# Performance work log

Measured on AMD Instinct MI355X. Metric: run time of the kernel, lower is better.

## Reference

```python
import jax, jax.numpy as jnp
from jax import lax
import numpy as np

D_COND = 48      # d_condition
K = 24           # n_bins
HID = 128        # hidden_dim
T = 10           # n_transforms
TAIL = 15.0      # tail_bound
B = 131072       # batch (contexts x samples flattened, as in sample())


def setup_inputs() -> dict:
    key = jax.random.key(0)
    ks = jax.random.split(key, 8)
    def w(k, shape, fan_in, gain=1.0):
        return (jax.random.normal(k, shape, jnp.float32) * (gain / np.sqrt(fan_in))).astype(jnp.float32)
    return {
        "z": jax.random.normal(ks[0], (B,), jnp.float32),
        "context": jax.random.normal(ks[1], (B, D_COND), jnp.float32),
        "W0": w(ks[2], (T, D_COND, HID), D_COND),
        "b0": jnp.zeros((T, HID), jnp.float32),
        "W1": w(ks[3], (T, HID, HID), HID),
        "b1": jnp.zeros((T, HID), jnp.float32),
        "W2": w(ks[4], (T, HID, HID), HID),
        "b2": jnp.zeros((T, HID), jnp.float32),
        "W3": w(ks[5], (T, HID, 3 * K + 1), HID, gain=0.1),
        "b3": jnp.zeros((T, 3 * K + 1), jnp.float32),
        "loc": jnp.float32(85.0),
        "scale": jnp.float32(5.0),
    }


def _spline_forward(x, widths, heights, derivs):
    # x: (B,); widths/heights: (B,K); derivs: (B,K+1)
    inside = (x >= -TAIL) & (x <= TAIL)
    cw = jnp.pad(jnp.cumsum(widths, -1), ((0, 0), (1, 0)), constant_values=-TAIL)   # (B,K+1)
    ch = jnp.pad(jnp.cumsum(heights, -1), ((0, 0), (1, 0)), constant_values=-TAIL)  # (B,K+1)
    # torch.searchsorted(cw[...,1:], x, right=False) == count of elems < x
    idx = jnp.clip(jnp.sum(cw[:, 1:] < x[:, None], axis=-1), 0, K - 1)
    take = lambda a, i: jnp.take_along_axis(a, i[:, None], axis=-1)[:, 0]
    w_k = take(widths, idx)
    h_k = take(heights, idx)
    cw_k = take(cw, idx)
    ch_k = take(ch, idx)
    d_k = take(derivs, idx)
    d_k1 = take(derivs, idx + 1)
    s = h_k / w_k
    xi = jnp.clip((x - cw_k) / w_k, 1e-6, 1.0 - 1e-6)
    one_m = 1.0 - xi
    numer = h_k * (s * xi * xi + d_k * xi * one_m)
    denom = s + (d_k + d_k1 - 2.0 * s) * xi * one_m
    y = ch_k + numer / denom
    dy_dxi = s * s * (d_k1 * xi * xi + 2.0 * s * xi * one_m + d_k * one_m * one_m) / (denom * denom)
    log_det = (jnp.log(jnp.maximum(dy_dxi, 1e-10))
               + jnp.log(jnp.maximum(h_k, 1e-10))
               - jnp.log(jnp.maximum(w_k, 1e-10)))
    y = jnp.where(inside, y, x)
    log_det = jnp.where(inside, log_det, 0.0)
    return y, log_det


def reference(z, context, W0, b0, W1, b1, W2, b2, W3, b3, loc, scale):
    def body(carry, p):
        zc, ld = carry
        w0, c0, w1, c1, w2, c2, w3, c3 = p
        h = jax.nn.silu(context @ w0 + c0)
        h = jax.nn.silu(h @ w1 + c1)
        h = jax.nn.silu(h @ w2 + c2)
        params = h @ w3 + c3                                   # (B, 3K+1)
        Wl, Hl, Dl = params[:, :K], params[:, K:2 * K], params[:, 2 * K:]
        widths = jax.nn.softmax(Wl, axis=-1) * (2.0 * TAIL)
        heights = jax.nn.softmax(Hl, axis=-1) * (2.0 * TAIL)
        derivs = jax.nn.softplus(Dl) + 1e-3
        y, l = _spline_forward(zc, widths, heights, derivs)
        return (y, ld + l), None

    (z_out, total_ld), _ = lax.scan(body, (z, jnp.zeros_like(z)),
                                    (W0, b0, W1, b1, W2, b2, W3, b3))
    s = jnp.maximum(scale, 0.1)
    temp_f = z_out * s + loc   # _unstandardize, as in sample()
    return temp_f, total_ld
```

## Files before the change

kernel.cpp:

```cpp
#include <hip/hip_runtime.h>
#include <hip/hip_bf16.h>

#define DCOND 48
#define KBINS 24
#define HID 128
#define TSTEPS 10
#define NPAR 73
#define TAILF 15.0f

typedef __attribute__((ext_vector_type(8))) short v8s;
typedef __attribute__((ext_vector_type(4))) float f32x4;
typedef __attribute__((ext_vector_type(4))) unsigned u32x4;

__device__ __forceinline__ short f2bf(float f) {
    __hip_bfloat16 h = __float2bfloat16(f);
    return __builtin_bit_cast(short, h);
}
__device__ __forceinline__ float bf2f(short s) {
    unsigned u = ((unsigned)(unsigned short)s) << 16;
    return __builtin_bit_cast(float, u);
}
__device__ __forceinline__ float silu_f(float v) {
    return __fdividef(v, 1.0f + __expf(-v));
}

__device__ __forceinline__ unsigned cvt_pk(float a, float b) {
    unsigned r;
    asm("v_cvt_pk_bf16_f32 %0, %1, %2" : "=v"(r) : "v"(a), "v"(b));
    return r;
}

__device__ __forceinline__ void split8(f32x4 a0, f32x4 a1, v8s& hi, v8s& lo) {
    unsigned h0 = cvt_pk(a0[0], a0[1]);
    unsigned h1 = cvt_pk(a0[2], a0[3]);
    unsigned h2 = cvt_pk(a1[0], a1[1]);
    unsigned h3 = cvt_pk(a1[2], a1[3]);
    float l0 = a0[0] - __builtin_bit_cast(float, h0 << 16);
    float l1 = a0[1] - __builtin_bit_cast(float, h0 & 0xffff0000u);
    float l2 = a0[2] - __builtin_bit_cast(float, h1 << 16);
    float l3 = a0[3] - __builtin_bit_cast(float, h1 & 0xffff0000u);
    float l4 = a1[0] - __builtin_bit_cast(float, h2 << 16);
    float l5 = a1[1] - __builtin_bit_cast(float, h2 & 0xffff0000u);
    float l6 = a1[2] - __builtin_bit_cast(float, h3 << 16);
    float l7 = a1[3] - __builtin_bit_cast(float, h3 & 0xffff0000u);
    unsigned q0 = cvt_pk(l0, l1);
    unsigned q1 = cvt_pk(l2, l3);
    unsigned q2 = cvt_pk(l4, l5);
    unsigned q3 = cvt_pk(l6, l7);
    hi = __builtin_bit_cast(v8s, (u32x4){h0, h1, h2, h3});
    lo = __builtin_bit_cast(v8s, (u32x4){q0, q1, q2, q3});
}

__global__ void prep_w(const float* __restrict__ W0, const float* __restrict__ W1,
                       const float* __restrict__ W2, const float* __restrict__ W3,
                       short* __restrict__ ws)
{
    int g = blockIdx.x * 256 + threadIdx.x;
    if (g >= TSTEPS * 102400) return;
    int t = g / 102400;
    int o = g % 102400;

    int base, NT, Kreal, Nreal, Nstr;
    const float* W;
    if (o < 16384)      { base = 0;     NT = 8; Kreal = 48;  Nreal = 128; Nstr = 128;  W = W0 + (size_t)t * DCOND * HID; }
    else if (o < 49152) { base = 16384; NT = 8; Kreal = 128; Nreal = 128; Nstr = 128;  W = W1 + (size_t)t * HID * HID; }
    else if (o < 81920) { base = 49152; NT = 8; Kreal = 128; Nreal = 128; Nstr = 128;  W = W2 + (size_t)t * HID * HID; }
    else                { base = 81920; NT = 5; Kreal = 128; Nreal = 73;  Nstr = NPAR; W = W3 + (size_t)t * HID * NPAR; }

    int r     = o - base;
    int psz   = 2 * NT * 512;
    int kc    = r / psz;
    int rem   = r % psz;
    int plane = rem / (NT * 512);
    int e     = rem % (NT * 512);
    int nt = e >> 9;
    int ln = (e >> 3) & 63;
    int j  = e & 7;
    int k  = kc * 32 + (ln >> 4) * 8 + j;
    int n  = nt * 16 + (ln & 15);

    float v = 0.0f;
    if (k < Kreal && n < Nreal) v = W[(size_t)k * Nstr + n];
    short hi = f2bf(v);
    ws[(size_t)t * 102400 + o] = plane ? f2bf(v - bf2f(hi)) : hi;
}

#define MBLK 64
#define NTHR 256

template<int SHORTS>
__device__ __forceinline__ void stage_piece(const short* __restrict__ g,
                                            short* lds, int tid)
{
    constexpr int R = (SHORTS + 2047) / 2048;
    const int wuni = (tid >> 6) << 9;
    #pragma unroll
    for (int i = 0; i < R; ++i) {
        const int so = i * 2048 + tid * 8;
        if ((SHORTS % 2048 == 0) || so < SHORTS)
            __builtin_amdgcn_global_load_lds(
                (const __attribute__((address_space(1))) void*)(g + so),
                (__attribute__((address_space(3))) void*)(lds + i * 2048 + wuni),
                16, 0, 0);
    }
}

template<int NT>
__device__ __forceinline__ void init_acc(f32x4* acc, const float* __restrict__ bias,
                                         int nreal, int lane)
{
    const int ncol = lane & 15;
    #pragma unroll
    for (int nt = 0; nt < NT; ++nt) {
        const int n = nt * 16 + ncol;
        const float bv = (n < nreal) ? bias[n] : 0.0f;
        acc[nt] = (f32x4){bv, bv, bv, bv};
    }
}

template<int NT>
__device__ __forceinline__ void mfma_piece(f32x4* acc, const short* __restrict__ buf,
                                           v8s ah, v8s al, int lane)
{
    const short* bb = buf + lane * 8;
    #pragma unroll
    for (int nt = 0; nt < NT; ++nt) {
        v8s bh = *(const v8s*)(bb + nt * 512);
        v8s bl = *(const v8s*)(bb + (NT + nt) * 512);
        acc[nt] = __builtin_amdgcn_mfma_f32_16x16x32_bf16(ah, bh, acc[nt], 0, 0, 0);
        acc[nt] = __builtin_amdgcn_mfma_f32_16x16x32_bf16(al, bh, acc[nt], 0, 0, 0);
        acc[nt] = __builtin_amdgcn_mfma_f32_16x16x32_bf16(ah, bl, acc[nt], 0, 0, 0);
    }
}

template<int NT, bool ACT>
__device__ __forceinline__ void cwrite(const f32x4* acc, float* __restrict__ Hlds,
                                       int lane, int wave)
{
    const int ncol  = lane & 15;
    const int crow0 = wave * 16 + (lane >> 4) * 4;
    #pragma unroll
    for (int nt = 0; nt < NT; ++nt) {
        #pragma unroll
        for (int r = 0; r < 4; ++r) {
            const int row = crow0 + r;
            const int sw  = (row & 7) << 4;
            float v = acc[nt][r];
            if (ACT) v = silu_f(v);
            *(float*)((char*)Hlds + row * 512 + ((((nt * 16 + ncol)) * 4) ^ sw)) = v;
        }
    }
}

__device__ __forceinline__ void a_split4(const float* __restrict__ Hlds,
                                         int arow, int asw, int lane,
                                         v8s (&ah)[4], v8s (&al)[4])
{
    const int kg = (lane >> 4) * 8;
    const char* hr = (const char*)Hlds + arow * 512;
    #pragma unroll
    for (int kc = 0; kc < 4; ++kc) {
        const int kb = (kc * 32 + kg) * 4;
        f32x4 a0 = *(const f32x4*)(hr + (kb ^ asw));
        f32x4 a1 = *(const f32x4*)(hr + ((kb + 16) ^ asw));
        split8(a0, a1, ah[kc], al[kc]);
    }
}

__global__ __launch_bounds__(NTHR, 2)
void nsf_mfma(const float* __restrict__ z_g, const float* __restrict__ ctx_g,
              const float* __restrict__ b0g, const float* __restrict__ b1g,
              const float* __restrict__ b2g, const float* __restrict__ b3g,
              const float* __restrict__ locp, const float* __restrict__ sclp,
              const short* __restrict__ wsW, float* __restrict__ out, int B)
{
    __shared__ float Hlds[MBLK * 128];
    __shared__ short CtxH[MBLK * 64];
    __shared__ short CtxL[MBLK * 64];
    __shared__ short Wbuf[2][8192];
    const int tid  = threadIdx.x;
    const int lane = tid & 63, wave = tid >> 6;
    const int blk  = blockIdx.x;

    stage_piece<8192>(wsW, Wbuf[0], tid);

    {
        const int row = tid >> 2, q = tid & 3;
        const int sw  = (row & 7) << 4;
        v8s h0, l0, h1, l1;
        if (q < 3) {
            int gs = blk * MBLK + row;
            if (gs > B - 1) gs = B - 1;
            const float* cg = ctx_g + (size_t)gs * DCOND + q * 16;
            f32x4 c0 = *(const f32x4*)cg;
            f32x4 c1 = *(const f32x4*)(cg + 4);
            f32x4 c2 = *(const f32x4*)(cg + 8);
            f32x4 c3 = *(const f32x4*)(cg + 12);
            split8(c0, c1, h0, l0);
            split8(c2, c3, h1, l1);
        } else {
            #pragma unroll
            for (int u = 0; u < 8; ++u) { h0[u] = 0; l0[u] = 0; h1[u] = 0; l1[u] = 0; }
        }
        char* ph = (char*)CtxH + row * 128;
        char* pl = (char*)CtxL + row * 128;
        *(v8s*)(ph + ((q * 32)      ^ sw)) = h0;
        *(v8s*)(ph + ((q * 32 + 16) ^ sw)) = h1;
        *(v8s*)(pl + ((q * 32)      ^ sw)) = l0;
        *(v8s*)(pl + ((q * 32 + 16) ^ sw)) = l1;
    }

    float x = 0.0f, ld = 0.0f;
    if (lane < 16) {
        int gid = blk * MBLK + wave * 16 + lane;
        if (gid > B - 1) gid = B - 1;
        x = z_g[gid];
    }

    __syncthreads();
    int cur = 0;

    const int arow = wave * 16 + (lane & 15);
    const int asw  = (arow & 7) << 4;

    v8s ah[4], al[4];
    f32x4 acc[8];

#define SLOT(STAGE_SHORTS, STAGE_SRC, NT_, AH, AL)                         \
    stage_piece<STAGE_SHORTS>((STAGE_SRC), Wbuf[cur ^ 1], tid);            \
    mfma_piece<NT_>(acc, Wbuf[cur], (AH), (AL), lane);

    #pragma unroll 1
    for (int t = 0; t < TSTEPS; ++t) {
        const short* ws0 = wsW + (size_t)t * 102400;
        const short* wsn = wsW + (size_t)((t + 1) % TSTEPS) * 102400;
        const float* b0 = b0g + t * HID;
        const float* b1 = b1g + t * HID;
        const float* b2 = b2g + t * HID;
        const float* b3 = b3g + t * NPAR;

        {
            const char* ph = (const char*)CtxH + arow * 128;
            const char* pl = (const char*)CtxL + arow * 128;
            const int kg2 = (lane >> 4) * 16;
            ah[0] = *(const v8s*)(ph + ((kg2)      ^ asw));
            al[0] = *(const v8s*)(pl + ((kg2)      ^ asw));
            ah[1] = *(const v8s*)(ph + ((64 + kg2) ^ asw));
            al[1] = *(const v8s*)(pl + ((64 + kg2) ^ asw));
        }
        init_acc<8>(acc, b0, HID, lane);
        SLOT(8192, ws0 + 8192,  8, ah[0], al[0]);  __syncthreads(); cur ^= 1;
        SLOT(8192, ws0 + 16384, 8, ah[1], al[1]);
        cwrite<8, true>(acc, Hlds, lane, wave);
        a_split4(Hlds, arow, asw, lane, ah, al);
        __syncthreads(); cur ^= 1;

        init_acc<8>(acc, b1, HID, lane);
        SLOT(8192, ws0 + 24576, 8, ah[0], al[0]);  __syncthreads(); cur ^= 1;
        SLOT(8192, ws0 + 32768, 8, ah[1], al[1]);  __syncthreads(); cur ^= 1;
        SLOT(8192, ws0 + 40960, 8, ah[2], al[2]);  __syncthreads(); cur ^= 1;
        SLOT(8192, ws0 + 49152, 8, ah[3], al[3]);
        cwrite<8, true>(acc, Hlds, lane, wave);
        a_split4(Hlds, arow, asw, lane, ah, al);
        __syncthreads(); cur ^= 1;

        init_acc<8>(acc, b2, HID, lane);
        SLOT(8192, ws0 + 57344, 8, ah[0], al[0]);  __syncthreads(); cur ^= 1;
        SLOT(8192, ws0 + 65536, 8, ah[1], al[1]);  __syncthreads(); cur ^= 1;
        SLOT(8192, ws0 + 73728, 8, ah[2], al[2]);  __syncthreads(); cur ^= 1;
        SLOT(5120, ws0 + 81920, 8, ah[3], al[3]);
        cwrite<8, true>(acc, Hlds, lane, wave);
        a_split4(Hlds, arow, asw, lane, ah, al);
        __syncthreads(); cur ^= 1;

        init_acc<5>(acc, b3, NPAR, lane);
        SLOT(5120, ws0 + 87040, 5, ah[0], al[0]);  __syncthreads(); cur ^= 1;
        SLOT(5120, ws0 + 92160, 5, ah[1], al[1]);  __syncthreads(); cur ^= 1;
        SLOT(5120, ws0 + 97280, 5, ah[2], al[2]);  __syncthreads(); cur ^= 1;
        SLOT(8192, wsn,         5, ah[3], al[3]);
        cwrite<5, false>(acc, Hlds, lane, wave);

        if (lane < 16) {
            const int srow = wave * 16 + lane;
            const char* hrow = (const char*)Hlds + srow * 512;
            const int sw = (srow & 7) << 4;

            float pw[KBINS], ph[KBINS];
            #pragma unroll
            for (int g = 0; g < 6; ++g) {
                f32x4 vw = *(const f32x4*)(hrow + ((g * 16) ^ sw));
                f32x4 vh = *(const f32x4*)(hrow + (((g + 6) * 16) ^ sw));
                #pragma unroll
                for (int u = 0; u < 4; ++u) { pw[g * 4 + u] = vw[u]; ph[g * 4 + u] = vh[u]; }
            }
            float mw = pw[0], mh = ph[0];
            #pragma unroll
            for (int i = 1; i < KBINS; ++i) { mw = fmaxf(mw, pw[i]); mh = fmaxf(mh, ph[i]); }
            float wsum = 0.0f, hsum = 0.0f;
            #pragma unroll
            for (int i = 0; i < KBINS; ++i) {
                pw[i] = __expf(pw[i] - mw); wsum += pw[i];
                ph[i] = __expf(ph[i] - mh); hsum += ph[i];
            }
            const float wmul = __fdividef(2.0f * TAILF, wsum);
            const float hmul = __fdividef(2.0f * TAILF, hsum);

            float cw = 0.0f, ch = 0.0f;
            float cwk = -TAILF, chk = -TAILF;
            float wk = pw[0] * wmul, hk = ph[0] * hmul;
            int idx = 0;
            #pragma unroll
            for (int i = 1; i < KBINS; ++i) {
                cw += pw[i - 1] * wmul;
                ch += ph[i - 1] * hmul;
                if (cw < x) {
                    cwk = cw; chk = ch;
                    wk = pw[i] * wmul; hk = ph[i] * hmul;
                    idx = i;
                }
            }
            float d0 = *(const float*)(hrow + (((2 * KBINS + idx) * 4) ^ sw));
            float d1 = *(const float*)(hrow + (((2 * KBINS + idx + 1) * 4) ^ sw));
            const float dk  = fmaxf(d0, 0.0f) + __logf(1.0f + __expf(-fabsf(d0))) + 0.001f;
            const float dk1 = fmaxf(d1, 0.0f) + __logf(1.0f + __expf(-fabsf(d1))) + 0.001f;

            const bool inside = (x >= -TAILF) && (x <= TAILF);
            const float sr = __fdividef(hk, wk);
            float xi = __fdividef(x - cwk, wk);
            xi = fminf(fmaxf(xi, 1e-6f), 1.0f - 1e-6f);
            const float om  = 1.0f - xi;
            const float xio = xi * om;
            const float numer = hk * (sr * xi * xi + dk * xio);
            const float denom = sr + (dk + dk1 - 2.0f * sr) * xio;
            const float y = chk + __fdividef(numer, denom);
            const float dyd = __fdividef(sr * sr * (dk1 * xi * xi + 2.0f * sr * xio + dk * om * om),
                                         denom * denom);
            const float lg = __logf(fmaxf(dyd, 1e-10f)) + __logf(fmaxf(hk, 1e-10f))
                           - __logf(fmaxf(wk, 1e-10f));
            x  = inside ? y : x;
            ld += inside ? lg : 0.0f;
        }
        __syncthreads(); cur ^= 1;
    }
#undef SLOT

    if (lane < 16) {
        const int gid = blk * MBLK + wave * 16 + lane;
        if (gid < B) {
            const float s = fmaxf(sclp[0], 0.1f);
            out[gid]     = fmaf(x, s, locp[0]);
            out[B + gid] = ld;
        }
    }
}

#define FBLK 256
template<int KIN, int WS, int NOUT, bool ACT>
__device__ __forceinline__ void dense_chunk(const float* __restrict__ W,
                                            const float* __restrict__ bias,
                                            int j0, const float (&hin)[KIN],
                                            float* __restrict__ sb, int tid)
{
    #pragma unroll 1
    for (int jj = 0; jj < NOUT; jj += 8) {
        const int j = j0 + jj;
        float a[8];
        #pragma unroll
        for (int u = 0; u < 8; ++u) a[u] = bias[j + u];
        #pragma unroll
        for (int k = 0; k < KIN; ++k) {
            const float* w = W + k * WS + j;
            const float hk = hin[k];
            #pragma unroll
            for (int u = 0; u < 8; ++u) a[u] = fmaf(hk, w[u], a[u]);
        }
        #pragma unroll
        for (int u = 0; u < 8; ++u) {
            float v = ACT ? silu_f(a[u]) : a[u];
            sb[(jj + u) * FBLK + tid] = v;
        }
    }
}

__global__ __launch_bounds__(FBLK, 2)
void nsf_fwd_slow(const float* __restrict__ z_g, const float* __restrict__ ctx_g,
                  const float* __restrict__ W0g, const float* __restrict__ b0g,
                  const float* __restrict__ W1g, const float* __restrict__ b1g,
                  const float* __restrict__ W2g, const float* __restrict__ b2g,
                  const float* __restrict__ W3g, const float* __restrict__ b3g,
                  const float* __restrict__ locp, const float* __restrict__ sclp,
                  float* __restrict__ out, int B)
{
    __shared__ float sbuf[64 * FBLK];
    const int tid = threadIdx.x;
    const int gid = blockIdx.x * FBLK + tid;
    if (gid >= B) return;
    float x = z_g[gid], ld = 0.0f;
    #pragma unroll 1
    for (int t = 0; t < TSTEPS; ++t) {
        asm volatile("" ::: "memory");
        const float* W0 = W0g + (size_t)t * DCOND * HID;
        const float* b0 = b0g + (size_t)t * HID;
        const float* W1 = W1g + (size_t)t * HID * HID;
        const float* b1 = b1g + (size_t)t * HID;
        const float* W2 = W2g + (size_t)t * HID * HID;
        const float* b2 = b2g + (size_t)t * HID;
        const float* W3 = W3g + (size_t)t * HID * NPAR;
        const float* b3 = b3g + (size_t)t * NPAR;
        float ctx[DCOND];
        #pragma unroll
        for (int k = 0; k < DCOND; ++k) ctx[k] = ctx_g[(size_t)gid * DCOND + k];
        float h[HID];
        dense_chunk<DCOND, HID, 64, true>(W0, b0, 0, ctx, sbuf, tid);
        #pragma unroll
        for (int j = 0; j < 64; ++j) h[j] = sbuf[j * FBLK + tid];
        dense_chunk<DCOND, HID, 64, true>(W0, b0, 64, ctx, sbuf, tid);
        #pragma unroll
        for (int j = 0; j < 64; ++j) h[64 + j] = sbuf[j * FBLK + tid];
        #pragma unroll 1
        for (int l = 0; l < 2; ++l) {
            const float* W  = (l == 0) ? W1 : W2;
            const float* bb = (l == 0) ? b1 : b2;
            float hlo[64];
            dense_chunk<HID, HID, 64, true>(W, bb, 0, h, sbuf, tid);
            #pragma unroll
            for (int j = 0; j < 64; ++j) hlo[j] = sbuf[j * FBLK + tid];
            dense_chunk<HID, HID, 64, true>(W, bb, 64, h, sbuf, tid);
            #pragma unroll
            for (int j = 0; j < 64; ++j) h[64 + j] = sbuf[j * FBLK + tid];
            #pragma unroll
            for (int j = 0; j < 64; ++j) h[j] = hlo[j];
        }
        float p[NPAR];
        dense_chunk<HID, NPAR, 64, false>(W3, b3, 0, h, sbuf, tid);
        #pragma unroll
        for (int j = 0; j < 64; ++j) p[j] = sbuf[j * FBLK + tid];
        dense_chunk<HID, NPAR, 8, false>(W3, b3, 64, h, sbuf, tid);
        #pragma unroll
        for (int j = 0; j < 8; ++j) p[64 + j] = sbuf[j * FBLK + tid];
        {
            float a = b3[72];
            #pragma unroll
            for (int k = 0; k < HID; ++k) a = fmaf(h[k], W3[k * NPAR + 72], a);
            p[72] = a;
        }
        float mw = p[0];
        #pragma unroll
        for (int i = 1; i < KBINS; ++i) mw = fmaxf(mw, p[i]);
        float we[KBINS]; float wsum = 0.0f;
        #pragma unroll
        for (int i = 0; i < KBINS; ++i) { we[i] = __expf(p[i] - mw); wsum += we[i]; }
        const float wmul = __fdividef(2.0f * TAILF, wsum);
        float mh = p[KBINS];
        #pragma unroll
        for (int i = 1; i < KBINS; ++i) mh = fmaxf(mh, p[KBINS + i]);
        float he[KBINS]; float hsum = 0.0f;
        #pragma unroll
        for (int i = 0; i < KBINS; ++i) { he[i] = __expf(p[KBINS + i] - mh); hsum += he[i]; }
        const float hmul = __fdividef(2.0f * TAILF, hsum);
        float dvv[KBINS + 1];
        #pragma unroll
        for (int i = 0; i <= KBINS; ++i) {
            float xd = p[2 * KBINS + i];
            dvv[i] = fmaxf(xd, 0.0f) + __logf(1.0f + __expf(-fabsf(xd))) + 0.001f;
        }
        float cw = 0.0f, ch = 0.0f, cwk = -TAILF, chk = -TAILF;
        float wk = we[0] * wmul, hk = he[0] * hmul, dk = dvv[0], dk1 = dvv[1];
        #pragma unroll
        for (int i = 1; i < KBINS; ++i) {
            cw += we[i - 1] * wmul;
            ch += he[i - 1] * hmul;
            if (cw < x) {
                cwk = cw; chk = ch;
                wk = we[i] * wmul; hk = he[i] * hmul;
                dk = dvv[i]; dk1 = dvv[i + 1];
            }
        }
        const bool inside = (x >= -TAILF) && (x <= TAILF);
        const float sr = __fdividef(hk, wk);
        float xi = __fdividef(x - cwk, wk);
        xi = fminf(fmaxf(xi, 1e-6f), 1.0f - 1e-6f);
        const float om  = 1.0f - xi;
        const float xio = xi * om;
        const float numer = hk * (sr * xi * xi + dk * xio);
        const float denom = sr + (dk + dk1 - 2.0f * sr) * xio;
        const float y = chk + __fdividef(numer, denom);
        const float dyd = __fdividef(sr * sr * (dk1 * xi * xi + 2.0f * sr * xio + dk * om * om),
                                     denom * denom);
        const float lg = __logf(fmaxf(dyd, 1e-10f)) + __logf(fmaxf(hk, 1e-10f))
                       - __logf(fmaxf(wk, 1e-10f));
        x  = inside ? y : x;
        ld += inside ? lg : 0.0f;
    }
    const float s = fmaxf(sclp[0], 0.1f);
    out[gid]     = fmaf(x, s, locp[0]);
    out[B + gid] = ld;
}

extern "C" void kernel_launch(void* const* d_in, const int* in_sizes, int n_in,
                              void* d_out, int out_size, void* d_ws, size_t ws_size,
                              hipStream_t stream) {
    const float* z    = (const float*)d_in[0];
    const float* ctx  = (const float*)d_in[1];
    const float* W0   = (const float*)d_in[2];
    const float* b0   = (const float*)d_in[3];
    const float* W1   = (const float*)d_in[4];
    const float* b1   = (const float*)d_in[5];
    const float* W2   = (const float*)d_in[6];
    const float* b2   = (const float*)d_in[7];
    const float* W3   = (const float*)d_in[8];
    const float* b3   = (const float*)d_in[9];
    const float* loc  = (const float*)d_in[10];
    const float* scl  = (const float*)d_in[11];
    float* out = (float*)d_out;
    const int B = in_sizes[0];

    const size_t ws_need = (size_t)TSTEPS * 102400 * sizeof(short);
    if (ws_size < ws_need) {
        const int nblk = (B + FBLK - 1) / FBLK;
        hipLaunchKernelGGL(nsf_fwd_slow, dim3(nblk), dim3(FBLK), 0, stream,
                           z, ctx, W0, b0, W1, b1, W2, b2, W3, b3, loc, scl, out, B);
        return;
    }

    short* ws = (short*)d_ws;
    const int prep_total = TSTEPS * 102400;
    hipLaunchKernelGGL(prep_w, dim3((prep_total + 255) / 256), dim3(256), 0, stream,
                       W0, W1, W2, W3, ws);

    const int nblk = (B + MBLK - 1) / MBLK;
    hipLaunchKernelGGL(nsf_mfma, dim3(nblk), dim3(NTHR), 0, stream,
                       z, ctx, b0, b1, b2, b3, loc, scl, ws, out, B);
}
```

Before: 678.1 us.

## Halve block rows and split N across wave pairs for higher occupancy

The row tile per block drops from 64 to 32. Each pair of waves now shares a 16-row M tile and splits the N columns in half, so every wave keeps 4 accumulators instead of 8. The weight staging buffer shrinks to 4096 shorts per stage and launch bounds ask for 4 blocks per CU, aiming at more resident blocks and fewer registers per thread. The cost is twice as many weight loads from global memory per sample, many more __syncthreads barriers with smaller pieces per stage, and an uneven N split in the last layer (4 tiles against 1).

```diff
diff --git a/kernel.cpp b/kernel.cpp
--- a/kernel.cpp
+++ b/kernel.cpp
@@ -85,7 +85,7 @@
     ws[(size_t)t * 102400 + o] = plane ? f2bf(v - bf2f(hi)) : hi;
 }
 
-#define MBLK 64
+#define MBLK 32
 #define NTHR 256
 
 template<int SHORTS>
@@ -105,69 +105,7 @@
     }
 }
 
-template<int NT>
-__device__ __forceinline__ void init_acc(f32x4* acc, const float* __restrict__ bias,
-                                         int nreal, int lane)
-{
-    const int ncol = lane & 15;
-    #pragma unroll
-    for (int nt = 0; nt < NT; ++nt) {
-        const int n = nt * 16 + ncol;
-        const float bv = (n < nreal) ? bias[n] : 0.0f;
-        acc[nt] = (f32x4){bv, bv, bv, bv};
-    }
-}
-
-template<int NT>
-__device__ __forceinline__ void mfma_piece(f32x4* acc, const short* __restrict__ buf,
-                                           v8s ah, v8s al, int lane)
-{
-    const short* bb = buf + lane * 8;
-    #pragma unroll
-    for (int nt = 0; nt < NT; ++nt) {
-        v8s bh = *(const v8s*)(bb + nt * 512);
-        v8s bl = *(const v8s*)(bb + (NT + nt) * 512);
-        acc[nt] = __builtin_amdgcn_mfma_f32_16x16x32_bf16(ah, bh, acc[nt], 0, 0, 0);
-        acc[nt] = __builtin_amdgcn_mfma_f32_16x16x32_bf16(al, bh, acc[nt], 0, 0, 0);
-        acc[nt] = __builtin_amdgcn_mfma_f32_16x16x32_bf16(ah, bl, acc[nt], 0, 0, 0);
-    }
-}
-
-template<int NT, bool ACT>
-__device__ __forceinline__ void cwrite(const f32x4* acc, float* __restrict__ Hlds,
-                                       int lane, int wave)
-{
-    const int ncol  = lane & 15;
-    const int crow0 = wave * 16 + (lane >> 4) * 4;
-    #pragma unroll
-    for (int nt = 0; nt < NT; ++nt) {
-        #pragma unroll
-        for (int r = 0; r < 4; ++r) {
-            const int row = crow0 + r;
-            const int sw  = (row & 7) << 4;
-            float v = acc[nt][r];
-            if (ACT) v = silu_f(v);
-            *(float*)((char*)Hlds + row * 512 + ((((nt * 16 + ncol)) * 4) ^ sw)) = v;
-        }
-    }
-}
-
-__device__ __forceinline__ void a_split4(const float* __restrict__ Hlds,
-                                         int arow, int asw, int lane,
-                                         v8s (&ah)[4], v8s (&al)[4])
-{
-    const int kg = (lane >> 4) * 8;
-    const char* hr = (const char*)Hlds + arow * 512;
-    #pragma unroll
-    for (int kc = 0; kc < 4; ++kc) {
-        const int kb = (kc * 32 + kg) * 4;
-        f32x4 a0 = *(const f32x4*)(hr + (kb ^ asw));
-        f32x4 a1 = *(const f32x4*)(hr + ((kb + 16) ^ asw));
-        split8(a0, a1, ah[kc], al[kc]);
-    }
-}
-
-__global__ __launch_bounds__(NTHR, 2)
+__global__ __launch_bounds__(NTHR, 4)
 void nsf_mfma(const float* __restrict__ z_g, const float* __restrict__ ctx_g,
               const float* __restrict__ b0g, const float* __restrict__ b1g,
               const float* __restrict__ b2g, const float* __restrict__ b3g,
@@ -177,111 +115,137 @@
     __shared__ float Hlds[MBLK * 128];
     __shared__ short CtxH[MBLK * 64];
     __shared__ short CtxL[MBLK * 64];
-    __shared__ short Wbuf[2][8192];
+    __shared__ short Wbuf[2][4096];
     const int tid  = threadIdx.x;
     const int lane = tid & 63, wave = tid >> 6;
+    const int mt   = wave >> 1, h = wave & 1;
     const int blk  = blockIdx.x;
 
-    stage_piece<8192>(wsW, Wbuf[0], tid);
+    stage_piece<4096>(wsW, Wbuf[0], tid);
 
     {
-        const int row = tid >> 2, q = tid & 3;
+        const int row = tid >> 3, q = tid & 7;
         const int sw  = (row & 7) << 4;
-        v8s h0, l0, h1, l1;
-        if (q < 3) {
+        v8s ch_, cl_;
+        if (q < 6) {
             int gs = blk * MBLK + row;
             if (gs > B - 1) gs = B - 1;
-            const float* cg = ctx_g + (size_t)gs * DCOND + q * 16;
+            const float* cg = ctx_g + (size_t)gs * DCOND + q * 8;
             f32x4 c0 = *(const f32x4*)cg;
             f32x4 c1 = *(const f32x4*)(cg + 4);
-            f32x4 c2 = *(const f32x4*)(cg + 8);
-            f32x4 c3 = *(const f32x4*)(cg + 12);
-            split8(c0, c1, h0, l0);
-            split8(c2, c3, h1, l1);
+            split8(c0, c1, ch_, cl_);
         } else {
             #pragma unroll
-            for (int u = 0; u < 8; ++u) { h0[u] = 0; l0[u] = 0; h1[u] = 0; l1[u] = 0; }
-        }
-        char* ph = (char*)CtxH + row * 128;
-        char* pl = (char*)CtxL + row * 128;
-        *(v8s*)(ph + ((q * 32)      ^ sw)) = h0;
-        *(v8s*)(ph + ((q * 32 + 16) ^ sw)) = h1;
-        *(v8s*)(pl + ((q * 32)      ^ sw)) = l0;
-        *(v8s*)(pl + ((q * 32 + 16) ^ sw)) = l1;
-    }
-
+            for (int u = 0; u < 8; ++u) { ch_[u] = 0; cl_[u] = 0; }
+        }
+        *(v8s*)((char*)CtxH + row * 128 + ((q * 16) ^ sw)) = ch_;
+        *(v8s*)((char*)CtxL + row * 128 + ((q * 16) ^ sw)) = cl_;
+    }
+
+    const int srow = mt * 16 + h * 8 + (lane & 7);
     float x = 0.0f, ld = 0.0f;
-    if (lane < 16) {
-        int gid = blk * MBLK + wave * 16 + lane;
+    if (lane < 8) {
+        int gid = blk * MBLK + srow;
         if (gid > B - 1) gid = B - 1;
         x = z_g[gid];
     }
 
+    const int arow  = mt * 16 + (lane & 15);
+    const int asw   = (arow & 7) << 4;
+    const int kg2   = (lane >> 4) * 16;
+    const int kgH   = (lane >> 4) * 32;
+    const int ncol  = lane & 15;
+    const int crow0 = mt * 16 + (lane >> 4) * 4;
+    const int nt0   = h * 4;
+    const int nt3   = h ? 4 : 0;
+    const int nw3   = h ? 1 : 4;
+
+    v8s ah[4], al[4];
+    f32x4 acc[4];
+    int cur = 0;
+
     __syncthreads();
-    int cur = 0;
-
-    const int arow = wave * 16 + (lane & 15);
-    const int asw  = (arow & 7) << 4;
-
-    v8s ah[4], al[4];
-    f32x4 acc[8];
-
-#define SLOT(STAGE_SHORTS, STAGE_SRC, NT_, AH, AL)                         \
-    stage_piece<STAGE_SHORTS>((STAGE_SRC), Wbuf[cur ^ 1], tid);            \
-    mfma_piece<NT_>(acc, Wbuf[cur], (AH), (AL), lane);
+
+#define STAGE(PTR, SZ) stage_piece<SZ>((PTR), Wbuf[cur ^ 1], tid)
+#define MH(KC, N0, NW) { const short* bb_ = Wbuf[cur] + (N0) * 512 + lane * 8;   \
+    _Pragma("unroll") for (int i_ = 0; i_ < 4; ++i_) if (i_ < (NW)) {            \
+      v8s b_ = *(const v8s*)(bb_ + i_ * 512);                                    \
+      acc[i_] = __builtin_amdgcn_mfma_f32_16x16x32_bf16(ah[KC], b_, acc[i_],0,0,0); \
+      acc[i_] = __builtin_amdgcn_mfma_f32_16x16x32_bf16(al[KC], b_, acc[i_],0,0,0); } }
+#define ML(KC, N0, NW) { const short* bb_ = Wbuf[cur] + (N0) * 512 + lane * 8;   \
+    _Pragma("unroll") for (int i_ = 0; i_ < 4; ++i_) if (i_ < (NW)) {            \
+      v8s b_ = *(const v8s*)(bb_ + i_ * 512);                                    \
+      acc[i_] = __builtin_amdgcn_mfma_f32_16x16x32_bf16(ah[KC], b_, acc[i_],0,0,0); } }
+#define INITACC(BIAS, NREAL, N0, NW)                                             \
+    _Pragma("unroll") for (int i_ = 0; i_ < 4; ++i_) if (i_ < (NW)) {            \
+      const int n_ = ((N0) + i_) * 16 + ncol;                                    \
+      const float bv_ = (n_ < (NREAL)) ? (BIAS)[n_] : 0.0f;                      \
+      acc[i_] = (f32x4){bv_, bv_, bv_, bv_}; }
+#define CW(ACT, N0, NW)                                                          \
+    _Pragma("unroll") for (int i_ = 0; i_ < 4; ++i_) if (i_ < (NW)) {            \
+      const int n_ = ((N0) + i_) * 16 + ncol;                                    \
+      _Pragma("unroll") for (int r_ = 0; r_ < 4; ++r_) {                         \
+        const int row_ = crow0 + r_; const int sw_ = (row_ & 7) << 4;            \
+        float v_ = acc[i_][r_]; if (ACT) v_ = silu_f(v_);                        \
+        *(float*)((char*)Hlds + row_ * 512 + ((n_ * 4) ^ sw_)) = v_; } }
+#define ASPLIT { const char* hr_ = (const char*)Hlds + arow * 512;               \
+    _Pragma("unroll") for (int kc_ = 0; kc_ < 4; ++kc_) {                        \
+      const int kb_ = kc_ * 128 + kgH;                                           \
+      f32x4 a0_ = *(const f32x4*)(hr_ + (kb_ ^ asw));                            \
+      f32x4 a1_ = *(const f32x4*)(hr_ + ((kb_ + 16) ^ asw));                     \
+      split8(a0_, a1_, ah[kc_], al[kc_]); } }
+#define BAR __syncthreads(); cur ^= 1
 
     #pragma unroll 1
     for (int t = 0; t < TSTEPS; ++t) {
         const short* ws0 = wsW + (size_t)t * 102400;
         const short* wsn = wsW + (size_t)((t + 1) % TSTEPS) * 102400;
-        const float* b0 = b0g + t * HID;
-        const float* b1 = b1g + t * HID;
-        const float* b2 = b2g + t * HID;
-        const float* b3 = b3g + t * NPAR;
 
         {
             const char* ph = (const char*)CtxH + arow * 128;
             const char* pl = (const char*)CtxL + arow * 128;
-            const int kg2 = (lane >> 4) * 16;
             ah[0] = *(const v8s*)(ph + ((kg2)      ^ asw));
             al[0] = *(const v8s*)(pl + ((kg2)      ^ asw));
             ah[1] = *(const v8s*)(ph + ((64 + kg2) ^ asw));
             al[1] = *(const v8s*)(pl + ((64 + kg2) ^ asw));
         }
-        init_acc<8>(acc, b0, HID, lane);
-        SLOT(8192, ws0 + 8192,  8, ah[0], al[0]);  __syncthreads(); cur ^= 1;
-        SLOT(8192, ws0 + 16384, 8, ah[1], al[1]);
-        cwrite<8, true>(acc, Hlds, lane, wave);
-        a_split4(Hlds, arow, asw, lane, ah, al);
-        __syncthreads(); cur ^= 1;
-
-        init_acc<8>(acc, b1, HID, lane);
-        SLOT(8192, ws0 + 24576, 8, ah[0], al[0]);  __syncthreads(); cur ^= 1;
-        SLOT(8192, ws0 + 32768, 8, ah[1], al[1]);  __syncthreads(); cur ^= 1;
-        SLOT(8192, ws0 + 40960, 8, ah[2], al[2]);  __syncthreads(); cur ^= 1;
-        SLOT(8192, ws0 + 49152, 8, ah[3], al[3]);
-        cwrite<8, true>(acc, Hlds, lane, wave);
-        a_split4(Hlds, arow, asw, lane, ah, al);
-        __syncthreads(); cur ^= 1;
-
-        init_acc<8>(acc, b2, HID, lane);
-        SLOT(8192, ws0 + 57344, 8, ah[0], al[0]);  __syncthreads(); cur ^= 1;
-        SLOT(8192, ws0 + 65536, 8, ah[1], al[1]);  __syncthreads(); cur ^= 1;
-        SLOT(8192, ws0 + 73728, 8, ah[2], al[2]);  __syncthreads(); cur ^= 1;
-        SLOT(5120, ws0 + 81920, 8, ah[3], al[3]);
-        cwrite<8, true>(acc, Hlds, lane, wave);
-        a_split4(Hlds, arow, asw, lane, ah, al);
-        __syncthreads(); cur ^= 1;
-
-        init_acc<5>(acc, b3, NPAR, lane);
-        SLOT(5120, ws0 + 87040, 5, ah[0], al[0]);  __syncthreads(); cur ^= 1;
-        SLOT(5120, ws0 + 92160, 5, ah[1], al[1]);  __syncthreads(); cur ^= 1;
-        SLOT(5120, ws0 + 97280, 5, ah[2], al[2]);  __syncthreads(); cur ^= 1;
-        SLOT(8192, wsn,         5, ah[3], al[3]);
-        cwrite<5, false>(acc, Hlds, lane, wave);
-
-        if (lane < 16) {
-            const int srow = wave * 16 + lane;
+        INITACC(b0g + t * HID, HID, nt0, 4);
+        STAGE(ws0 +  4096, 4096); MH(0, nt0, 4); BAR;
+        STAGE(ws0 +  8192, 4096); ML(0, nt0, 4); BAR;
+        STAGE(ws0 + 12288, 4096); MH(1, nt0, 4); BAR;
+        STAGE(ws0 + 16384, 4096); ML(1, nt0, 4); CW(true, nt0, 4); BAR;
+
+        ASPLIT; INITACC(b1g + t * HID, HID, nt0, 4);
+        STAGE(ws0 + 20480, 4096); MH(0, nt0, 4); BAR;
+        STAGE(ws0 + 24576, 4096); ML(0, nt0, 4); BAR;
+        STAGE(ws0 + 28672, 4096); MH(1, nt0, 4); BAR;
+        STAGE(ws0 + 32768, 4096); ML(1, nt0, 4); BAR;
+        STAGE(ws0 + 36864, 4096); MH(2, nt0, 4); BAR;
+        STAGE(ws0 + 40960, 4096); ML(2, nt0, 4); BAR;
+        STAGE(ws0 + 45056, 4096); MH(3, nt0, 4); BAR;
+        STAGE(ws0 + 49152, 4096); ML(3, nt0, 4); CW(true, nt0, 4); BAR;
+
+        ASPLIT; INITACC(b2g + t * HID, HID, nt0, 4);
+        STAGE(ws0 + 53248, 4096); MH(0, nt0, 4); BAR;
+        STAGE(ws0 + 57344, 4096); ML(0, nt0, 4); BAR;
+        STAGE(ws0 + 61440, 4096); MH(1, nt0, 4); BAR;
+        STAGE(ws0 + 65536, 4096); ML(1, nt0, 4); BAR;
+        STAGE(ws0 + 69632, 4096); MH(2, nt0, 4); BAR;
+        STAGE(ws0 + 73728, 4096); ML(2, nt0, 4); BAR;
+        STAGE(ws0 + 77824, 4096); MH(3, nt0, 4); BAR;
+        STAGE(ws0 + 81920, 2560); ML(3, nt0, 4); CW(true, nt0, 4); BAR;
+
+        ASPLIT; INITACC(b3g + t * NPAR, NPAR, nt3, nw3);
+        STAGE(ws0 + 84480, 2560); MH(0, nt3, nw3); BAR;
+        STAGE(ws0 + 87040, 2560); ML(0, nt3, nw3); BAR;
+        STAGE(ws0 + 89600, 2560); MH(1, nt3, nw3); BAR;
+        STAGE(ws0 + 92160, 2560); ML(1, nt3, nw3); BAR;
+        STAGE(ws0 + 94720, 2560); MH(2, nt3, nw3); BAR;
+        STAGE(ws0 + 97280, 2560); ML(2, nt3, nw3); BAR;
+        STAGE(ws0 + 99840, 2560); MH(3, nt3, nw3); BAR;
+        STAGE(wsn,         4096); ML(3, nt3, nw3); CW(false, nt3, nw3); BAR;
+
+        if (lane < 8) {
             const char* hrow = (const char*)Hlds + srow * 512;
             const int sw = (srow & 7) << 4;
 
@@ -340,12 +304,17 @@
             x  = inside ? y : x;
             ld += inside ? lg : 0.0f;
         }
-        __syncthreads(); cur ^= 1;
-    }
-#undef SLOT
-
-    if (lane < 16) {
-        const int gid = blk * MBLK + wave * 16 + lane;
+    }
+#undef STAGE
+#undef MH
+#undef ML
+#undef INITACC
+#undef CW
+#undef ASPLIT
+#undef BAR
+
+    if (lane < 8) {
+        const int gid = blk * MBLK + srow;
         if (gid < B) {
             const float s = fmaxf(sclp[0], 0.1f);
             out[gid]     = fmaf(x, s, locp[0]);
```

After: 804.9 us. 1.19x slower.
